# Performance work log

Measured on AMD Instinct MI355X. Metric: run time of the kernel, lower is better.

Reference implementation:

```python
import jax, jax.numpy as jnp
import numpy as np
import math

N_EMBD = 1024
N_HEADS = 16
B, T = 4, 2048

def setup_inputs() -> dict:
    key = jax.random.key(0)
    k1, k2, k3 = jax.random.split(key, 3)
    x = jax.random.normal(k1, (B, T, N_EMBD), dtype=jnp.float32)
    scale = 1.0 / math.sqrt(N_EMBD)
    W_attn = jax.random.normal(k2, (N_EMBD, 3 * N_EMBD), dtype=jnp.float32) * scale
    W_proj = jax.random.normal(k3, (N_EMBD, N_EMBD), dtype=jnp.float32) * scale
    return {"x": x, "W_attn": W_attn, "W_proj": W_proj}

def reference(x, W_attn, W_proj):
    Bb, Tt, C = x.shape
    hd = C // N_HEADS
    qkv = x @ W_attn  # [B,T,3C]
    q, k, v = jnp.split(qkv, 3, axis=-1)
    # [B,H,T,hd]
    q = q.reshape(Bb, Tt, N_HEADS, hd).transpose(0, 2, 1, 3)
    k = k.reshape(Bb, Tt, N_HEADS, hd).transpose(0, 2, 1, 3)
    v = v.reshape(Bb, Tt, N_HEADS, hd).transpose(0, 2, 1, 3)
    att = jnp.einsum('bhqd,bhkd->bhqk', q, k) * (1.0 / math.sqrt(hd))
    mask = jnp.tril(jnp.ones((Tt, Tt), dtype=bool))
    att = jnp.where(mask[None, None], att, -jnp.inf)
    att = jax.nn.softmax(att, axis=-1)
    out = jnp.einsum('bhqk,bhkd->bhqd', att, v)
    out = out.transpose(0, 2, 1, 3).reshape(Bb, Tt, C)
    return out @ W_proj
```

## Files before the change

kernel.cpp:

```cpp
#include <hip/hip_runtime.h>
#include <cstddef>
#include <cstdint>

typedef __attribute__((ext_vector_type(8))) _Float16 half8;
typedef __attribute__((ext_vector_type(4))) _Float16 half4;
typedef __attribute__((ext_vector_type(4))) float f32x4;
typedef __attribute__((ext_vector_type(16))) float f32x16;

#define N_EMBD 1024
#define N_HEADS 16
#define BATCH 4
#define SEQ 2048
#define C3 3072
#define HD 64

__device__ inline uint32_t pk2(float x, float y) {
    auto h2 = __builtin_amdgcn_cvt_pkrtz(x, y);
    uint32_t u;
    __builtin_memcpy(&u, &h2, 4);
    return u;
}

__device__ inline void swap32(uint32_t& a, uint32_t& b) {
    asm volatile("v_permlane32_swap_b32 %0, %1" : "+v"(a), "+v"(b));
}

__device__ inline float exp2_hw(float x) {
    float r;
    asm("v_exp_f32 %0, %1" : "=v"(r) : "v"(x));
    return r;
}

__device__ inline void transpose_tile(const float* __restrict__ in, _Float16* __restrict__ out,
                                      int R, int Ncols, int bx, int by, int tx, int ty) {
    __shared__ float tile[32][33];
    int n0 = bx * 32, r0 = by * 32;
#pragma unroll
    for (int i = 0; i < 32; i += 8)
        tile[ty + i][tx] = in[(size_t)(r0 + ty + i) * Ncols + n0 + tx];
    __syncthreads();
#pragma unroll
    for (int i = 0; i < 32; i += 8)
        out[(size_t)(n0 + ty + i) * R + r0 + tx] = (_Float16)tile[tx][ty + i];
}

__global__ void prep_kernel(const float* __restrict__ x, _Float16* __restrict__ xh,
                            const float* __restrict__ Wa, _Float16* __restrict__ WaT,
                            const float* __restrict__ Wp, _Float16* __restrict__ WpT) {
    const int bid = blockIdx.x;
    const int tx = threadIdx.x & 31, ty = threadIdx.x >> 5;
    if (bid < 8192) {
        int i = (bid * 256 + threadIdx.x) * 4;
        float4 v = *(const float4*)(x + i);
        half4 h;
        h[0] = (_Float16)v.x; h[1] = (_Float16)v.y; h[2] = (_Float16)v.z; h[3] = (_Float16)v.w;
        *(half4*)(xh + i) = h;
    } else if (bid < 8192 + 3072) {
        int v = bid - 8192;
        transpose_tile(Wa, WaT, N_EMBD, C3, v % 96, v / 96, tx, ty);
    } else {
        int v = bid - 8192 - 3072;
        transpose_tile(Wp, WpT, N_EMBD, N_EMBD, v % 32, v / 32, tx, ty);
    }
}

__global__ void transpose_v(const _Float16* __restrict__ qkv, _Float16* __restrict__ vT) {
    __shared__ _Float16 tile[32][36];
    int t0 = blockIdx.x * 32;
    int bhd = blockIdx.y;
    int bh = bhd >> 1, dh = bhd & 1;
    int b = bh >> 4, h = bh & 15;
    int tx = threadIdx.x, ty = threadIdx.y;
#pragma unroll
    for (int i = 0; i < 32; i += 8)
        tile[ty + i][tx] = qkv[(size_t)(b * SEQ + t0 + ty + i) * C3 + 2 * N_EMBD + h * HD + dh * 32 + tx];
    __syncthreads();
#pragma unroll
    for (int i = 0; i < 32; i += 8)
        vT[((size_t)bh * HD + dh * 32 + ty + i) * SEQ + t0 + tx] = tile[tx][ty + i];
}

__device__ inline void store1(float* p, float v) { *p = v; }
__device__ inline void store1(_Float16* p, float v) { *p = (_Float16)v; }

template <typename OutT>
__global__ __launch_bounds__(512, 1) void gemm192(
    const _Float16* __restrict__ A, const _Float16* __restrict__ Bt,
    OutT* __restrict__ C, int M, int N, int K) {
    __shared__ _Float16 Al[2][256 * 64];
    __shared__ _Float16 Bl[2][192 * 64];
    const int tid = threadIdx.x;
    const int lane = tid & 63, wave = tid >> 6;
    const int l15 = lane & 15, l4 = lane >> 4;
    const int wm = wave >> 2, wn = wave & 3;

    const int nwg = gridDim.x, nbx = N / 192;
    int wg = blockIdx.x;
    if ((nwg & 7) == 0) { int cpx = nwg >> 3; wg = (wg & 7) * cpx + (wg >> 3); }
    const int row0 = (wg / nbx) * 256, col0 = (wg % nbx) * 192;
    const int TAU = K >> 6;

    const int srow = tid >> 3, su = tid & 7;
    const int usrc8 = (su ^ (srow & 7)) * 8;
    auto stageAu = [&](int unit, int ts) {
        __builtin_amdgcn_global_load_lds(
            (const __attribute__((address_space(1))) void*)(A + (size_t)(row0 + unit * 64 + srow) * K + ts * 64 + usrc8),
            (__attribute__((address_space(3))) void*)(&Al[ts & 1][unit * 64 * 64 + tid * 8]), 16, 0, 0);
    };
    auto stageBu = [&](int unit, int ts) {
        __builtin_amdgcn_global_load_lds(
            (const __attribute__((address_space(1))) void*)(Bt + (size_t)(col0 + unit * 64 + srow) * K + ts * 64 + usrc8),
            (__attribute__((address_space(3))) void*)(&Bl[ts & 1][unit * 64 * 64 + tid * 8]), 16, 0, 0);
    };
    auto stageTile = [&](int ts) {
        stageAu(0, ts); stageAu(1, ts); stageAu(2, ts); stageAu(3, ts);
        stageBu(0, ts); stageBu(1, ts); stageBu(2, ts);
    };

    f32x4 acc[8][3] = {};
    stageTile(0); stageTile(1);
    asm volatile("s_waitcnt vmcnt(7)" ::: "memory");
    __builtin_amdgcn_s_barrier();

    half8 a[4][2], b[3][2];
    for (int tau = 0; tau < TAU; ++tau) {
        const _Float16* Ab = &Al[tau & 1][0];
        const _Float16* Bb = &Bl[tau & 1][0];
        const bool t2 = (tau + 2 < TAU);

#pragma unroll
        for (int m = 0; m < 4; ++m)
#pragma unroll
            for (int ks = 0; ks < 2; ++ks) {
                int r = wm * 128 + m * 16 + l15;
                a[m][ks] = *(const half8*)(Ab + r * 64 + (((ks * 4 + l4) ^ (r & 7)) * 8));
            }
#pragma unroll
        for (int n = 0; n < 3; ++n)
#pragma unroll
            for (int ks = 0; ks < 2; ++ks) {
                int r = wn * 48 + n * 16 + l15;
                b[n][ks] = *(const half8*)(Bb + r * 64 + (((ks * 4 + l4) ^ (r & 7)) * 8));
            }
        __builtin_amdgcn_s_barrier();
        __builtin_amdgcn_s_setprio(1);
#pragma unroll
        for (int m = 0; m < 4; ++m)
#pragma unroll
            for (int n = 0; n < 2; ++n)
#pragma unroll
                for (int ks = 0; ks < 2; ++ks)
                    acc[m][n] = __builtin_amdgcn_mfma_f32_16x16x32_f16(a[m][ks], b[n][ks], acc[m][n], 0, 0, 0);
        __builtin_amdgcn_s_setprio(0);
        __builtin_amdgcn_s_barrier();

        if (t2) { stageBu(0, tau + 2); stageBu(1, tau + 2); stageBu(2, tau + 2); }
        __builtin_amdgcn_s_barrier();
        __builtin_amdgcn_s_setprio(1);
#pragma unroll
        for (int m = 0; m < 4; ++m)
#pragma unroll
            for (int ks = 0; ks < 2; ++ks)
                acc[m][2] = __builtin_amdgcn_mfma_f32_16x16x32_f16(a[m][ks], b[2][ks], acc[m][2], 0, 0, 0);
        __builtin_amdgcn_s_setprio(0);
        __builtin_amdgcn_s_barrier();

#pragma unroll
        for (int m = 0; m < 4; ++m)
#pragma unroll
            for (int ks = 0; ks < 2; ++ks) {
                int r = wm * 128 + 64 + m * 16 + l15;
                a[m][ks] = *(const half8*)(Ab + r * 64 + (((ks * 4 + l4) ^ (r & 7)) * 8));
            }
        if (t2) { stageAu(0, tau + 2); stageAu(2, tau + 2); }
        __builtin_amdgcn_s_barrier();
        __builtin_amdgcn_s_setprio(1);
#pragma unroll
        for (int m = 0; m < 4; ++m)
#pragma unroll
            for (int n = 0; n < 2; ++n)
#pragma unroll
                for (int ks = 0; ks < 2; ++ks)
                    acc[4 + m][n] = __builtin_amdgcn_mfma_f32_16x16x32_f16(a[m][ks], b[n][ks], acc[4 + m][n], 0, 0, 0);
        __builtin_amdgcn_s_setprio(0);
        __builtin_amdgcn_s_barrier();

        if (t2) { stageAu(1, tau + 2); stageAu(3, tau + 2); }
        __builtin_amdgcn_s_barrier();
        __builtin_amdgcn_s_setprio(1);
#pragma unroll
        for (int m = 0; m < 4; ++m)
#pragma unroll
            for (int ks = 0; ks < 2; ++ks)
                acc[4 + m][2] = __builtin_amdgcn_mfma_f32_16x16x32_f16(a[m][ks], b[2][ks], acc[4 + m][2], 0, 0, 0);
        __builtin_amdgcn_s_setprio(0);
        if (tau <= TAU - 3) {
            asm volatile("s_waitcnt vmcnt(7)" ::: "memory");
        } else if (tau == TAU - 2) {
            asm volatile("s_waitcnt vmcnt(0)" ::: "memory");
        }
        __builtin_amdgcn_s_barrier();
    }

#pragma unroll
    for (int mi = 0; mi < 8; ++mi)
#pragma unroll
        for (int ni = 0; ni < 3; ++ni)
#pragma unroll
            for (int j = 0; j < 4; ++j) {
                int r = row0 + wm * 128 + (mi >> 2) * 64 + (mi & 3) * 16 + l4 * 4 + j;
                int c = col0 + wn * 48 + ni * 16 + l15;
                store1(C + (size_t)r * N + c, acc[mi][ni][j]);
            }
}

template <typename OutT>
__global__ __launch_bounds__(256, 2) void gemm_h(
    const _Float16* __restrict__ A, const _Float16* __restrict__ Bt,
    OutT* __restrict__ C, int M, int N, int K) {
    __shared__ _Float16 Al[3][128 * 32];
    __shared__ _Float16 Bl[3][128 * 32];
    const int tid = threadIdx.x;
    const int wave = tid >> 6, lane = tid & 63;
    const int l15 = lane & 15, l4 = lane >> 4;
    const int gx = gridDim.x;
    int lin = blockIdx.y * gx + blockIdx.x;
    int bcol, brow;
    if ((gx & 7) == 0) {
        int cpx = gx >> 3;
        int xcd = lin & 7;
        int idx = lin >> 3;
        bcol = xcd * cpx + idx % cpx;
        brow = idx / cpx;
    } else { bcol = blockIdx.x; brow = blockIdx.y; }
    const int row0 = brow * 128, col0 = bcol * 128;
    const int wm = wave >> 1, wn = wave & 1;
    const int TAU = K >> 5;

    auto stageT = [&](int ts, int buf) {
#pragma unroll
        for (int i = 0; i < 2; ++i) {
            int c = tid + 256 * i;
            int r = c >> 2, c8 = (c & 3) * 8;
            __builtin_amdgcn_global_load_lds(
                (const __attribute__((address_space(1))) void*)(A + (size_t)(row0 + r) * K + ts * 32 + c8),
                (__attribute__((address_space(3))) void*)(&Al[buf][(size_t)(wave * 64 + 256 * i) * 8]),
                16, 0, 0);
        }
#pragma unroll
        for (int i = 0; i < 2; ++i) {
            int c = tid + 256 * i;
            int r = c >> 2, c8 = (c & 3) * 8;
            __builtin_amdgcn_global_load_lds(
                (const __attribute__((address_space(1))) void*)(Bt + (size_t)(col0 + r) * K + ts * 32 + c8),
                (__attribute__((address_space(3))) void*)(&Bl[buf][(size_t)(wave * 64 + 256 * i) * 8]),
                16, 0, 0);
        }
    };

    f32x4 acc[4][4] = {};
    stageT(0, 0); stageT(1, 1);
    asm volatile("s_waitcnt vmcnt(4)" ::: "memory");
    __builtin_amdgcn_s_barrier();

    int cur = 0;
    for (int t = 0; t < TAU; ++t) {
        int sb = cur + 2; if (sb >= 3) sb -= 3;
        if (t + 2 < TAU) stageT(t + 2, sb);
        half8 a[4], b[4];
#pragma unroll
        for (int m = 0; m < 4; ++m)
            a[m] = *(const half8*)(&Al[cur][(wm * 64 + m * 16 + l15) * 32 + l4 * 8]);
#pragma unroll
        for (int n = 0; n < 4; ++n)
            b[n] = *(const half8*)(&Bl[cur][(wn * 64 + n * 16 + l15) * 32 + l4 * 8]);
        __builtin_amdgcn_s_setprio(1);
#pragma unroll
        for (int m = 0; m < 4; ++m)
#pragma unroll
            for (int n = 0; n < 4; ++n)
                acc[m][n] = __builtin_amdgcn_mfma_f32_16x16x32_f16(a[m], b[n], acc[m][n], 0, 0, 0);
        __builtin_amdgcn_s_setprio(0);
        if (t + 2 < TAU) {
            asm volatile("s_waitcnt vmcnt(4)" ::: "memory");
        } else if (t + 1 < TAU) {
            asm volatile("s_waitcnt vmcnt(0)" ::: "memory");
        }
        __builtin_amdgcn_s_barrier();
        ++cur; if (cur == 3) cur = 0;
    }
#pragma unroll
    for (int m = 0; m < 4; ++m)
#pragma unroll
        for (int n = 0; n < 4; ++n)
#pragma unroll
            for (int j = 0; j < 4; ++j) {
                int r = row0 + wm * 64 + m * 16 + l4 * 4 + j;
                int cc = col0 + wn * 64 + n * 16 + l15;
                store1(C + (size_t)r * N + cc, acc[m][n][j]);
            }
}

__global__ __launch_bounds__(256, 3) void attn_kernel(const _Float16* __restrict__ qkv,
                                                      const _Float16* __restrict__ vT,
                                                      _Float16* __restrict__ ao) {
    const int bid = blockIdx.x;
    const int pairp = bid >> 6;
    const int bh = bid & 63;
    const int b = bh >> 4, h = bh & 15;
    const int tid = threadIdx.x, lane = tid & 63;
    const int wave = tid >> 6;
    const int l31 = lane & 31, L = lane >> 5;

    __shared__ _Float16 Kl[3][64 * 64];
    __shared__ _Float16 Vl[3][64 * 64];
    __shared__ float l_s[4][32];

    const float qscale = 0.125f * 1.44269504089f;
    const float NEGC = -4.0f * 1.44269504089f;

    auto stage = [&](int t, int buf) {
#pragma unroll
        for (int i = 0; i < 2; ++i) {
            int idx = tid + 256 * i;
            int key = idx >> 3;
            int d8 = ((idx & 7) ^ (key & 7)) * 8;
            __builtin_amdgcn_global_load_lds(
                (const __attribute__((address_space(1))) void*)(qkv + (size_t)(b * SEQ + t * 64 + key) * C3 + N_EMBD + h * HD + d8),
                (__attribute__((address_space(3))) void*)(&Kl[buf][idx * 8]), 16, 0, 0);
        }
#pragma unroll
        for (int i = 0; i < 2; ++i) {
            int idx = tid + 256 * i;
            int d = idx >> 3;
            int k8 = ((idx & 7) ^ (d & 7)) * 8;
            __builtin_amdgcn_global_load_lds(
                (const __attribute__((address_space(1))) void*)(vT + ((size_t)bh * HD + d) * SEQ + t * 64 + k8),
                (__attribute__((address_space(3))) void*)(&Vl[buf][idx * 8]), 16, 0, 0);
        }
    };

    const f32x16 cinit = (f32x16)(NEGC);

    for (int pass = 0; pass < 2; ++pass) {
        const int qt = pass ? (15 - pairp) : pairp;
        const int q0w = qt * 128 + wave * 32;
        const int q_g = q0w + l31;
        const int nt = 2 * qt + 2;

        stage(0, 0);
        stage(1, 1);

        half8 qb[4];
#pragma unroll
        for (int ks = 0; ks < 4; ++ks) {
            half8 v = *(const half8*)(qkv + (size_t)(b * SEQ + q_g) * C3 + h * HD + ks * 16 + L * 8);
#pragma unroll
            for (int e = 0; e < 8; ++e) v[e] = (_Float16)((float)v[e] * qscale);
            qb[ks] = v;
        }

        f32x16 o[2];
        o[0] = (f32x16)(0.f);
        o[1] = (f32x16)(0.f);
        float ls0 = 0.f, ls1 = 0.f, ls2 = 0.f, ls3 = 0.f;

        asm volatile("s_waitcnt vmcnt(4)" ::: "memory");
        __builtin_amdgcn_s_barrier();

        int cur = 0;
        for (int t = 0; t < nt; ++t) {
            const int kv0 = t * 64;
            int sb = cur + 2; if (sb >= 3) sb -= 3;
            if (t + 2 < nt) stage(t + 2, sb);

            if (kv0 <= q0w + 31) {
                const _Float16* Kb = &Kl[cur][0];
                const _Float16* Vb = &Vl[cur][0];
                f32x16 s[2];
                __builtin_amdgcn_s_setprio(1);
#pragma unroll
                for (int kb = 0; kb < 2; ++kb) {
                    const int key = kb * 32 + l31;
                    {
                        half8 kf = *(const half8*)(Kb + key * 64 + ((L ^ (key & 7)) * 8));
                        s[kb] = __builtin_amdgcn_mfma_f32_32x32x16_f16(kf, qb[0], cinit, 0, 0, 0);
                    }
#pragma unroll
                    for (int ks = 1; ks < 4; ++ks) {
                        half8 kf = *(const half8*)(Kb + key * 64 + (((ks * 2 + L) ^ (key & 7)) * 8));
                        s[kb] = __builtin_amdgcn_mfma_f32_32x32x16_f16(kf, qb[ks], s[kb], 0, 0, 0);
                    }
                }
                __builtin_amdgcn_s_setprio(0);
                const bool needmask = (kv0 + 63 > q0w);
#pragma unroll
                for (int kb = 0; kb < 2; ++kb) {
#pragma unroll
                    for (int r = 0; r < 16; ++r) {
                        float v = exp2_hw(s[kb][r]);
                        if (needmask) {
                            int key_g = kv0 + kb * 32 + (r & 3) + 8 * (r >> 2) + 4 * L;
                            v = (key_g > q_g) ? 0.f : v;
                        }
                        s[kb][r] = v;
                        if ((r & 3) == 0) ls0 += v;
                        else if ((r & 3) == 1) ls1 += v;
                        else if ((r & 3) == 2) ls2 += v;
                        else ls3 += v;
                    }
                }
                half8 paf[4];
#pragma unroll
                for (int kb = 0; kb < 2; ++kb)
#pragma unroll
                    for (int hf = 0; hf < 2; ++hf) {
                        const int bse = hf * 8;
                        uint32_t a0 = pk2(s[kb][bse + 0], s[kb][bse + 1]);
                        uint32_t b0 = pk2(s[kb][bse + 4], s[kb][bse + 5]);
                        swap32(a0, b0);
                        uint32_t a1 = pk2(s[kb][bse + 2], s[kb][bse + 3]);
                        uint32_t b1 = pk2(s[kb][bse + 6], s[kb][bse + 7]);
                        swap32(a1, b1);
                        uint32_t w[4] = {a0, a1, b0, b1};
                        __builtin_memcpy(&paf[kb * 2 + hf], w, 16);
                    }
                __builtin_amdgcn_s_setprio(1);
#pragma unroll
                for (int ks = 0; ks < 4; ++ks) {
#pragma unroll
                    for (int db = 0; db < 2; ++db) {
                        const int d = db * 32 + l31;
                        half8 vb = *(const half8*)(Vb + d * 64 + (((ks * 2 + L) ^ (d & 7)) * 8));
                        o[db] = __builtin_amdgcn_mfma_f32_32x32x16_f16(paf[ks], vb, o[db], 0, 0, 0);
                    }
                }
                __builtin_amdgcn_s_setprio(0);
            }

            if (t + 2 < nt) {
                asm volatile("s_waitcnt vmcnt(4)" ::: "memory");
            } else if (t + 1 < nt) {
                asm volatile("s_waitcnt vmcnt(0)" ::: "memory");
            }
            __builtin_amdgcn_s_barrier();
            ++cur; if (cur == 3) cur = 0;
        }

        float lrow = (ls0 + ls1) + (ls2 + ls3);
        lrow += __shfl_xor(lrow, 32, 64);
        l_s[wave][l31] = lrow;
        asm volatile("s_waitcnt lgkmcnt(0)" ::: "memory");
        __builtin_amdgcn_sched_barrier(0);
        float lq[16];
#pragma unroll
        for (int r = 0; r < 16; ++r)
            lq[r] = l_s[wave][(r & 3) + 8 * (r >> 2) + 4 * L];
        asm volatile("s_waitcnt lgkmcnt(0)" ::: "memory");
        __builtin_amdgcn_sched_barrier(0);
#pragma unroll
        for (int db = 0; db < 2; ++db)
#pragma unroll
            for (int r = 0; r < 16; ++r) {
                int qg = q0w + (r & 3) + 8 * (r >> 2) + 4 * L;
                ao[(size_t)(b * SEQ + qg) * N_EMBD + h * HD + db * 32 + l31] =
                    (_Float16)(o[db][r] / lq[r]);
            }
    }
}

extern "C" void kernel_launch(void* const* d_in, const int* in_sizes, int n_in,
                              void* d_out, int out_size, void* d_ws, size_t ws_size,
                              hipStream_t stream) {
    const float* x  = (const float*)d_in[0];
    const float* Wa = (const float*)d_in[1];
    const float* Wp = (const float*)d_in[2];
    float* out = (float*)d_out;

    const int M = BATCH * SEQ;
    _Float16* xh  = (_Float16*)d_ws;
    _Float16* WaT = xh + (size_t)M * N_EMBD;
    _Float16* WpT = WaT + (size_t)C3 * N_EMBD;
    _Float16* qkv = WpT + (size_t)N_EMBD * N_EMBD;
    _Float16* ao  = qkv + (size_t)M * C3;
    _Float16* vT  = xh;

    prep_kernel<<<dim3(8192 + 3072 + 1024), 256, 0, stream>>>(x, xh, Wa, WaT, Wp, WpT);

    gemm192<_Float16><<<dim3((M / 256) * (C3 / 192)), 512, 0, stream>>>(xh, WaT, qkv, M, C3, N_EMBD);

    dim3 tb(32, 8);
    transpose_v<<<dim3(SEQ / 32, BATCH * N_HEADS * 2), tb, 0, stream>>>(qkv, vT);

    attn_kernel<<<dim3(512), 256, 0, stream>>>(qkv, vT, ao);

    gemm_h<float><<<dim3(N_EMBD / 128, M / 128), 256, 0, stream>>>(ao, WpT, out, M, N_EMBD, N_EMBD);
}
```

Before: 182.2 us.

## Fuse V transpose into QKV GEMM epilogue and fold Q scale into weights

The QKV GEMM epilogue now writes the V columns transposed into a separate vT buffer through LDS staging, so the standalone transpose_v kernel launch is removed when the workspace is large enough. The softmax scale for Q is folded into the transposed W_attn during weight prep, which removes the per-element Q scaling in the attention kernel. The cost is extra LDS traffic and a barrier in the GEMM epilogue, plus a larger workspace requirement. Folding the scale into the weights before the fp16 conversion changes rounding slightly.

After: 168.1 us (median of 2 runs). 1.08x faster.

```diff
diff --git a/kernel.cpp b/kernel.cpp
--- a/kernel.cpp
+++ b/kernel.cpp
@@ -32,7 +32,8 @@
 }
 
 __device__ inline void transpose_tile(const float* __restrict__ in, _Float16* __restrict__ out,
-                                      int R, int Ncols, int bx, int by, int tx, int ty) {
+                                      int R, int Ncols, int bx, int by, int tx, int ty,
+                                      int scale_below, float scl) {
     __shared__ float tile[32][33];
     int n0 = bx * 32, r0 = by * 32;
 #pragma unroll
@@ -40,8 +41,12 @@
         tile[ty + i][tx] = in[(size_t)(r0 + ty + i) * Ncols + n0 + tx];
     __syncthreads();
 #pragma unroll
-    for (int i = 0; i < 32; i += 8)
-        out[(size_t)(n0 + ty + i) * R + r0 + tx] = (_Float16)tile[tx][ty + i];
+    for (int i = 0; i < 32; i += 8) {
+        int orow = n0 + ty + i;
+        float f = tile[tx][ty + i];
+        if (orow < scale_below) f *= scl;
+        out[(size_t)orow * R + r0 + tx] = (_Float16)f;
+    }
 }
 
 __global__ void prep_kernel(const float* __restrict__ x, _Float16* __restrict__ xh,
@@ -49,6 +54,7 @@
                             const float* __restrict__ Wp, _Float16* __restrict__ WpT) {
     const int bid = blockIdx.x;
     const int tx = threadIdx.x & 31, ty = threadIdx.x >> 5;
+    const float qscale = 0.125f * 1.44269504089f;
     if (bid < 8192) {
         int i = (bid * 256 + threadIdx.x) * 4;
         float4 v = *(const float4*)(x + i);
@@ -57,10 +63,10 @@
         *(half4*)(xh + i) = h;
     } else if (bid < 8192 + 3072) {
         int v = bid - 8192;
-        transpose_tile(Wa, WaT, N_EMBD, C3, v % 96, v / 96, tx, ty);
+        transpose_tile(Wa, WaT, N_EMBD, C3, v % 96, v / 96, tx, ty, N_EMBD, qscale);
     } else {
         int v = bid - 8192 - 3072;
-        transpose_tile(Wp, WpT, N_EMBD, N_EMBD, v % 32, v / 32, tx, ty);
+        transpose_tile(Wp, WpT, N_EMBD, N_EMBD, v % 32, v / 32, tx, ty, 0, 1.0f);
     }
 }
 
@@ -83,12 +89,12 @@
 __device__ inline void store1(float* p, float v) { *p = v; }
 __device__ inline void store1(_Float16* p, float v) { *p = (_Float16)v; }
 
-template <typename OutT>
 __global__ __launch_bounds__(512, 1) void gemm192(
     const _Float16* __restrict__ A, const _Float16* __restrict__ Bt,
-    OutT* __restrict__ C, int M, int N, int K) {
-    __shared__ _Float16 Al[2][256 * 64];
-    __shared__ _Float16 Bl[2][192 * 64];
+    _Float16* __restrict__ C, _Float16* __restrict__ vT, int M, int N, int K) {
+    __shared__ _Float16 smem[2 * 256 * 64 + 2 * 192 * 64];
+    _Float16* Al0 = smem;
+    _Float16* Bl0 = smem + 2 * 256 * 64;
     const int tid = threadIdx.x;
     const int lane = tid & 63, wave = tid >> 6;
     const int l15 = lane & 15, l4 = lane >> 4;
@@ -105,12 +111,12 @@
     auto stageAu = [&](int unit, int ts) {
         __builtin_amdgcn_global_load_lds(
             (const __attribute__((address_space(1))) void*)(A + (size_t)(row0 + unit * 64 + srow) * K + ts * 64 + usrc8),
-            (__attribute__((address_space(3))) void*)(&Al[ts & 1][unit * 64 * 64 + tid * 8]), 16, 0, 0);
+            (__attribute__((address_space(3))) void*)(Al0 + (ts & 1) * 16384 + unit * 4096 + tid * 8), 16, 0, 0);
     };
     auto stageBu = [&](int unit, int ts) {
         __builtin_amdgcn_global_load_lds(
             (const __attribute__((address_space(1))) void*)(Bt + (size_t)(col0 + unit * 64 + srow) * K + ts * 64 + usrc8),
-            (__attribute__((address_space(3))) void*)(&Bl[ts & 1][unit * 64 * 64 + tid * 8]), 16, 0, 0);
+            (__attribute__((address_space(3))) void*)(Bl0 + (ts & 1) * 12288 + unit * 4096 + tid * 8), 16, 0, 0);
     };
     auto stageTile = [&](int ts) {
         stageAu(0, ts); stageAu(1, ts); stageAu(2, ts); stageAu(3, ts);
@@ -124,8 +130,8 @@
 
     half8 a[4][2], b[3][2];
     for (int tau = 0; tau < TAU; ++tau) {
-        const _Float16* Ab = &Al[tau & 1][0];
-        const _Float16* Bb = &Bl[tau & 1][0];
+        const _Float16* Ab = Al0 + (tau & 1) * 16384;
+        const _Float16* Bb = Bl0 + (tau & 1) * 12288;
         const bool t2 = (tau + 2 < TAU);
 
 #pragma unroll
@@ -202,16 +208,43 @@
         __builtin_amdgcn_s_barrier();
     }
 
+    const int vlo = 2 * N_EMBD;
+    const bool fuseV = (vT != nullptr) && (col0 + 192 > vlo);
+    _Float16* vbuf = smem;
 #pragma unroll
     for (int mi = 0; mi < 8; ++mi)
 #pragma unroll
-        for (int ni = 0; ni < 3; ++ni)
-#pragma unroll
-            for (int j = 0; j < 4; ++j) {
-                int r = row0 + wm * 128 + (mi >> 2) * 64 + (mi & 3) * 16 + l4 * 4 + j;
-                int c = col0 + wn * 48 + ni * 16 + l15;
-                store1(C + (size_t)r * N + c, acc[mi][ni][j]);
-            }
+        for (int ni = 0; ni < 3; ++ni) {
+            int c = col0 + wn * 48 + ni * 16 + l15;
+            int rb = wm * 128 + (mi >> 2) * 64 + (mi & 3) * 16 + l4 * 4;
+            if ((vT != nullptr) && c >= vlo) {
+                if (fuseV) {
+                    half4 hv;
+#pragma unroll
+                    for (int j = 0; j < 4; ++j) hv[j] = (_Float16)acc[mi][ni][j];
+                    *(half4*)(&vbuf[(c - col0) * 264 + rb]) = hv;
+                }
+            } else {
+#pragma unroll
+                for (int j = 0; j < 4; ++j)
+                    store1(C + (size_t)(row0 + rb + j) * N + c, acc[mi][ni][j]);
+            }
+        }
+    if (fuseV) {
+        __syncthreads();
+        const int vc0 = (col0 > vlo) ? col0 : vlo;
+        const int W = col0 + 192 - vc0;
+        const int nch = W * 32;
+        const int bB = row0 >> 11;
+        const int t0 = row0 & 2047;
+        for (int ch = tid; ch < nch; ch += 512) {
+            int crow = ch >> 5, ck = ch & 31;
+            int c = vc0 + crow;
+            half8 hv = *(const half8*)(&vbuf[(c - col0) * 264 + ck * 8]);
+            int hh = (c - vlo) >> 6, dd = (c - vlo) & 63;
+            *(half8*)(&vT[((size_t)(bB * 16 + hh) * 64 + dd) * SEQ + t0 + ck * 8]) = hv;
+        }
+    }
 }
 
 template <typename OutT>
@@ -316,7 +349,6 @@
     __shared__ _Float16 Vl[3][64 * 64];
     __shared__ float l_s[4][32];
 
-    const float qscale = 0.125f * 1.44269504089f;
     const float NEGC = -4.0f * 1.44269504089f;
 
     auto stage = [&](int t, int buf) {
@@ -353,12 +385,8 @@
 
         half8 qb[4];
 #pragma unroll
-        for (int ks = 0; ks < 4; ++ks) {
-            half8 v = *(const half8*)(qkv + (size_t)(b * SEQ + q_g) * C3 + h * HD + ks * 16 + L * 8);
-#pragma unroll
-            for (int e = 0; e < 8; ++e) v[e] = (_Float16)((float)v[e] * qscale);
-            qb[ks] = v;
-        }
+        for (int ks = 0; ks < 4; ++ks)
+            qb[ks] = *(const half8*)(qkv + (size_t)(b * SEQ + q_g) * C3 + h * HD + ks * 16 + L * 8);
 
         f32x16 o[2];
         o[0] = (f32x16)(0.f);
@@ -483,14 +511,22 @@
     _Float16* WpT = WaT + (size_t)C3 * N_EMBD;
     _Float16* qkv = WpT + (size_t)N_EMBD * N_EMBD;
     _Float16* ao  = qkv + (size_t)M * C3;
-    _Float16* vT  = xh;
+    _Float16* vTn = ao + (size_t)M * N_EMBD;
+
+    const size_t need = ((size_t)M * N_EMBD * 3 + (size_t)C3 * N_EMBD +
+                         (size_t)N_EMBD * N_EMBD + (size_t)M * C3) * sizeof(_Float16);
+    const bool fused = (ws_size >= need);
+    _Float16* vT = fused ? vTn : xh;
 
     prep_kernel<<<dim3(8192 + 3072 + 1024), 256, 0, stream>>>(x, xh, Wa, WaT, Wp, WpT);
 
-    gemm192<_Float16><<<dim3((M / 256) * (C3 / 192)), 512, 0, stream>>>(xh, WaT, qkv, M, C3, N_EMBD);
-
-    dim3 tb(32, 8);
-    transpose_v<<<dim3(SEQ / 32, BATCH * N_HEADS * 2), tb, 0, stream>>>(qkv, vT);
+    gemm192<<<dim3((M / 256) * (C3 / 192)), 512, 0, stream>>>(
+        xh, WaT, qkv, fused ? vT : nullptr, M, C3, N_EMBD);
+
+    if (!fused) {
+        dim3 tb(32, 8);
+        transpose_v<<<dim3(SEQ / 32, BATCH * N_HEADS * 2), tb, 0, stream>>>(qkv, vT);
+    }
 
     attn_kernel<<<dim3(512), 256, 0, stream>>>(qkv, vT, ao);
 
```
